# Kernel optimization log

Hardware: AMD Instinct MI355X
Metric: run time of the kernel (lower is better)

## Reference

```python
import jax, jax.numpy as jnp
import numpy as np

EPS = 1e-5


def setup_inputs() -> dict:
    key = jax.random.key(0)
    ks = jax.random.split(key, 10)
    B, C, H, W = 4, 256, 64, 64
    x = jax.random.normal(ks[0], (B, C, H, W), dtype=jnp.float32)
    s = 1.0 / np.sqrt(C)
    inp = {
        "x": x,
        "gn_w": jnp.ones((C,), jnp.float32),
        "gn_b": jnp.zeros((C,), jnp.float32),
        "wq": jax.random.normal(ks[1], (C, C), jnp.float32) * s,
        "bq": jnp.zeros((C,), jnp.float32),
        "wk": jax.random.normal(ks[2], (C, C), jnp.float32) * s,
        "bk": jnp.zeros((C,), jnp.float32),
        "wv": jax.random.normal(ks[3], (C, C), jnp.float32) * s,
        "bv": jnp.zeros((C,), jnp.float32),
        "wo": jax.random.normal(ks[4], (C, C), jnp.float32) * s,
        "bo": jnp.zeros((C,), jnp.float32),
    }
    return inp


def _forward(x, gn_w, gn_b, wq, bq, wk, bk, wv, bv, wo, bo):
    B, C, H, W = x.shape
    G = C // 2  # num_groups = channels // 2 -> 2 channels per group
    # GroupNorm
    xg = x.reshape(B, G, C // G, H, W)
    mu = jnp.mean(xg, axis=(2, 3, 4), keepdims=True)
    var = jnp.var(xg, axis=(2, 3, 4), keepdims=True)
    hn = ((xg - mu) * jax.lax.rsqrt(var + EPS)).reshape(B, C, H, W)
    hn = hn * gn_w[None, :, None, None] + gn_b[None, :, None, None]
    # tokens: (B, N, C), N = H*W
    h = hn.transpose(0, 2, 3, 1).reshape(B, H * W, C)
    q = h @ wq.T + bq
    k = h @ wk.T + bk
    v = h @ wv.T + bv
    # full NxN attention, scaled by C^-0.5 (as in original)
    scores = jnp.einsum("bnc,bmc->bnm", q, k) * (C ** -0.5)
    attn = jax.nn.softmax(scores, axis=-1)
    h2 = jnp.einsum("bnm,bmc->bnc", attn, v)  # (B, N, C)
    # faithful replication of the original's layout-scrambling reshape:
    # (B,N,C) -> (B,H,W,C) -> permute (B,C,H,W) -> reshape (B,HW,C)
    h2 = h2.reshape(B, H, W, C).transpose(0, 3, 1, 2).reshape(B, H * W, C)
    out = (h2 @ wo.T + bo).reshape(B, C, H, W)
    return x + out


def reference(x, gn_w, gn_b, wq, bq, wk, bk, wv, bv, wo, bo):
    return _forward(x, gn_w, gn_b, wq, bq, wk, bk, wv, bv, wo, bo)
```

## Files before the change

### kernel.cpp

```cpp
#include <hip/hip_runtime.h>

typedef unsigned short u16;
typedef unsigned int   u32;
typedef __attribute__((ext_vector_type(8)))  short short8;
typedef __attribute__((ext_vector_type(4)))  float f32x4;
typedef __attribute__((ext_vector_type(16))) float f32x16;

#define DI __device__ __forceinline__

DI u16 f2bf(float f){
  u32 u = __builtin_bit_cast(u32, f);
  u += 0x7fffu + ((u >> 16) & 1u);
  return (u16)(u >> 16);
}

DI void gl_lds16(const void* g, void* l){
  __builtin_amdgcn_global_load_lds((const __attribute__((address_space(1))) void*)g,
                                   (__attribute__((address_space(3))) void*)l, 16, 0, 0);
}

DI f32x4 mfma16(short8 a, short8 b, f32x4 c){
  return __builtin_amdgcn_mfma_f32_16x16x32_bf16(a, b, c, 0, 0, 0);
}
DI f32x16 mfma32(short8 a, short8 b, f32x16 c){
  return __builtin_amdgcn_mfma_f32_32x32x16_bf16(a, b, c, 0, 0, 0);
}
DI f32x16 z16(){
  f32x16 v;
  #pragma unroll
  for (int i=0;i<16;i++) v[i]=0.f;
  return v;
}

union U8 { u32 u[4]; short8 s; };

#define OFF_WBF   0u
#define OFF_STATS (512u<<10)
#define OFF_HTOK  (1u<<20)
#define OFF_Q     ((1u<<20) + (8u<<20))
#define OFF_K     ((1u<<20) + (16u<<20))
#define OFF_VT    ((1u<<20) + (24u<<20))
#define OFF_H2T   OFF_Q
#define OFF_PART  ((1u<<20) + (32u<<20))
#define OFF_ML    ((1u<<20) + (96u<<20))

__global__ void k_prep(const float* w0, const float* w1, const float* w2, const float* w3, u16* wbf){
  const float* src = (blockIdx.y==0)?w0:(blockIdx.y==1)?w1:(blockIdx.y==2)?w2:w3;
  u16* d = wbf + blockIdx.y*65536;
  int i = (blockIdx.x*256 + threadIdx.x)*4;
  float4 v = *(const float4*)(src + i);
  u32 lo = (u32)f2bf(v.x) | ((u32)f2bf(v.y)<<16);
  u32 hi = (u32)f2bf(v.z) | ((u32)f2bf(v.w)<<16);
  *(uint2*)(d + i) = make_uint2(lo, hi);
}

__global__ void k_gnstats(const float* x, float2* stats){
  int bg = blockIdx.x;
  const float* p = x + (size_t)bg*8192;
  float s = 0.f, ss = 0.f;
  #pragma unroll
  for (int i=0;i<8;i++){
    float4 v = *(const float4*)(p + threadIdx.x*4 + i*1024);
    s  += v.x+v.y+v.z+v.w;
    ss += v.x*v.x + v.y*v.y + v.z*v.z + v.w*v.w;
  }
  #pragma unroll
  for (int off=1; off<64; off<<=1){ s += __shfl_xor(s, off, 64); ss += __shfl_xor(ss, off, 64); }
  __shared__ float as[4], aq[4];
  int w = threadIdx.x>>6;
  if ((threadIdx.x&63)==0){ as[w]=s; aq[w]=ss; }
  __syncthreads();
  if (threadIdx.x==0){
    s = as[0]+as[1]+as[2]+as[3]; ss = aq[0]+aq[1]+aq[2]+aq[3];
    float mu = s * (1.f/8192.f);
    float var = ss * (1.f/8192.f) - mu*mu;
    stats[bg] = make_float2(mu, rsqrtf(var + 1e-5f));
  }
}

__global__ void k_gnapply(const float* x, const float* gw, const float* gb,
                          const float2* stats, u16* htok){
  __shared__ u16 tile[64*256];
  int b = blockIdx.y, n0 = blockIdx.x*64, t = threadIdx.x;
  const float* xb = x + (size_t)b*1048576;
  #pragma unroll
  for (int p=0;p<4;p++){
    int c = p*64 + (t>>2);
    float2 st = stats[b*128 + (c>>1)];
    float scl = st.y * gw[c];
    float off = gb[c] - st.x*scl;
    const float* src = xb + (size_t)c*4096 + n0 + (t&3)*16;
    #pragma unroll
    for (int u2=0;u2<4;u2++){
      float4 v = *(const float4*)(src + u2*4);
      float vv[4] = {v.x,v.y,v.z,v.w};
      #pragma unroll
      for (int j=0;j<4;j++){
        int n = (t&3)*16 + u2*4 + j;
        int addr = n*512 + ((c*2) ^ ((n&7)<<4));
        *(u16*)((char*)tile + addr) = f2bf(vv[j]*scl + off);
      }
    }
  }
  __syncthreads();
  int n = t>>2, seg = t&3;
  char* dst = (char*)(htok + ((size_t)(b*4096 + n0 + n)*256 + seg*64));
  #pragma unroll
  for (int i=0;i<8;i++){
    int boff = n*512 + (((seg*128) + i*16) ^ ((n&7)<<4));
    *(uint4*)(dst + i*16) = *(const uint4*)((const char*)tile + boff);
  }
}

DI void gemm_v2(const u16* Ag, const u16* Wg, int row0, int t,
                u16* lds_a, f32x4 acc[4][4]){
  const int w = t>>6, l = t&63, lo = l&15, hi = l>>4;
  const char* Ab = (const char*)Ag + (size_t)row0*512;
  #pragma unroll
  for (int i=0;i<8;i++){
    int row = w*16 + i*2 + (l>>5);
    gl_lds16(Ab + row*512 + (((l&31)*16) ^ ((row&7)<<4)), lds_a + w*4096 + i*512);
  }
  __syncthreads();
  const char* Wb = (const char*)Wg;
  #pragma unroll
  for (int dk=0; dk<4; dk++){
    #pragma unroll
    for (int s=0;s<2;s++){
      short8 af[4], bf[4];
      #pragma unroll
      for (int cf=0;cf<4;cf++){
        int col = w*64 + cf*16 + lo;
        bf[cf] = *(const short8*)(Wb + (size_t)col*512 + dk*128 + s*64 + hi*16);
      }
      #pragma unroll
      for (int rg=0;rg<4;rg++){
        int row = rg*16 + lo;
        af[rg] = *(const short8*)((const char*)lds_a + row*512 + ((dk*128 + s*64 + hi*16) ^ ((row&7)<<4)));
      }
      #pragma unroll
      for (int rg=0;rg<4;rg++)
        #pragma unroll
        for (int cf=0;cf<4;cf++)
          acc[rg][cf] = mfma16(af[rg], bf[cf], acc[rg][cf]);
    }
  }
}

__global__ __launch_bounds__(256,2) void k_qkv(const u16* htok, const u16* wbf,
    const float* bq, const float* bk, const float* bv,
    u16* qo, u16* ko, u16* vt){
  __shared__ u16 lds_a[64*256];
  const int t = threadIdx.x, mode = blockIdx.y, row0 = blockIdx.x*64;
  const u16* W = wbf + mode*65536;
  const float* bias = (mode==0)?bq:((mode==1)?bk:bv);
  f32x4 acc[4][4];
  #pragma unroll
  for (int i=0;i<4;i++)
    #pragma unroll
    for (int j=0;j<4;j++) acc[i][j] = (f32x4){0.f,0.f,0.f,0.f};
  gemm_v2(htok, W, row0, t, lds_a, acc);
  const int w = t>>6, l = t&63, lo = l&15, hi = l>>4;
  if (mode < 2){
    float scl = (mode==0)? 0.09016844f : 1.0f;
    u16* dst = (mode==0)? qo : ko;
    #pragma unroll
    for (int rg=0;rg<4;rg++)
      #pragma unroll
      for (int cf=0;cf<4;cf++){
        int col = w*64 + cf*16 + lo;
        float bs = bias[col];
        #pragma unroll
        for (int r=0;r<4;r++){
          int grow = row0 + rg*16 + hi*4 + r;
          dst[(size_t)grow*256 + col] = f2bf((acc[rg][cf][r] + bs)*scl);
        }
      }
  } else {
    __syncthreads();
    #pragma unroll
    for (int rg=0;rg<4;rg++)
      #pragma unroll
      for (int cf=0;cf<4;cf++){
        int col = w*64 + cf*16 + lo;
        float bs = bias[col];
        ushort4 pk;
        pk.x = f2bf(acc[rg][cf][0]+bs); pk.y = f2bf(acc[rg][cf][1]+bs);
        pk.z = f2bf(acc[rg][cf][2]+bs); pk.w = f2bf(acc[rg][cf][3]+bs);
        int rl = rg*16 + hi*4;
        int addr = col*128 + ((rl*2) ^ ((col&7)<<4));
        *(ushort4*)((char*)lds_a + addr) = pk;
      }
    __syncthreads();
    int b = row0 >> 12, nb = row0 & 4095;
    #pragma unroll
    for (int p=0;p<8;p++){
      int c = p*32 + (t>>3), i = t&7;
      uint4 vd = *(const uint4*)((const char*)lds_a + c*128 + ((i*16) ^ ((c&7)<<4)));
      *(uint4*)((char*)vt + ((size_t)(b*256 + c)*4096 + nb)*2 + i*16) = vd;
    }
  }
}

__global__ __launch_bounds__(256,2) void k_out(const u16* h2t, const u16* wo,
    const float* bo, const float* x, float* out){
  __shared__ u16 lds_a[64*256];
  const int t = threadIdx.x, row0 = blockIdx.x*64;
  f32x4 acc[4][4];
  #pragma unroll
  for (int i=0;i<4;i++)
    #pragma unroll
    for (int j=0;j<4;j++) acc[i][j] = (f32x4){0.f,0.f,0.f,0.f};
  gemm_v2(h2t, wo, row0, t, lds_a, acc);
  const int w = t>>6, l = t&63, lo = l&15, hi = l>>4;
  #pragma unroll
  for (int rg=0;rg<4;rg++)
    #pragma unroll
    for (int cf=0;cf<4;cf++){
      int col = w*64 + cf*16 + lo;
      float bs = bo[col];
      #pragma unroll
      for (int r=0;r<4;r++){
        size_t flat = (size_t)(row0 + rg*16 + hi*4 + r)*256 + col;
        out[flat] = x[flat] + acc[rg][cf][r] + bs;
      }
    }
}

__global__ __launch_bounds__(512,2) void k_attn(const u16* q, const u16* k,
                                                const u16* vt, u16* part, float2* ml){
  __shared__ char smem[131072];
  const int t = threadIdx.x, w = t>>6, l = t&63;
  const int lq = l&31, h = l>>5;
  const int bid = blockIdx.x;
  const int x = bid&7, idx = bid>>3;
  const int combo = x*2 + (idx&1);
  const int b = combo>>2, ks = combo&3, qt = idx>>1;

  const char* kg = (const char*)k  + ((size_t)b*4096 + (size_t)ks*1024)*512;
  const char* vg = (const char*)vt + (size_t)b*2097152 + (size_t)ks*2048;

  short8 qf[16];
  {
    const char* qrow = (const char*)q + ((size_t)b*4096 + qt*256 + w*32 + lq)*512;
    #pragma unroll
    for (int dk=0;dk<16;dk++) qf[dk] = *(const short8*)(qrow + dk*32 + h*16);
  }

  f32x16 O[8];
  #pragma unroll
  for (int ct=0;ct<8;ct++) O[ct] = z16();
  float m_run = -1e30f, l_run = 0.f;

  auto stage = [&](int ti, int buf){
    #pragma unroll
    for (int sub=0; sub<2; ++sub){
      char* kd = smem + buf*32768 + sub*16384;
      char* vd = smem + 65536 + buf*32768 + sub*16384;
      #pragma unroll
      for (int j=0;j<2;j++){
        int key = w*4 + j*2 + h;
        gl_lds16(kg + (size_t)(ti*64 + sub*32 + key)*512 + (((l&31)*16) ^ ((key&7)<<4)),
                 kd + (w*2+j)*1024);
      }
      #pragma unroll
      for (int j=0;j<2;j++){
        int c = w*32 + j*16 + (l>>2);
        gl_lds16(vg + (size_t)c*8192 + ti*128 + sub*64 + (((l&3)*16) ^ (((l>>3)&3)<<4)),
                 vd + (w*2+j)*1024);
      }
    }
  };

  auto smpv = [&](const f32x16& S, const char* vbuf){
    float pmax = S[0];
    #pragma unroll
    for (int r=1;r<16;r++) pmax = fmaxf(pmax, S[r]);
    pmax = fmaxf(pmax, __shfl_xor(pmax, 32, 64));
    if (__any(pmax > m_run + 8.f)){
      float mn = fmaxf(m_run, pmax);
      float sclq = exp2f(m_run - mn);
      m_run = mn;
      l_run *= sclq;
      #pragma unroll
      for (int r=0;r<16;r++){
        float sr = __shfl(sclq, (r&3)+8*(r>>2)+4*h, 64);
        #pragma unroll
        for (int ct=0;ct<8;ct++) O[ct][r] *= sr;
      }
    }
    float p[16]; float ps = 0.f;
    #pragma unroll
    for (int r=0;r<16;r++){ p[r] = exp2f(S[r] - m_run); ps += p[r]; }
    l_run += ps + __shfl_xor(ps, 32, 64);
    u32 pk[8];
    #pragma unroll
    for (int j=0;j<8;j++){
      u32 u0 = __builtin_bit_cast(u32, p[2*j]);
      u32 u1 = __builtin_bit_cast(u32, p[2*j+1]);
      pk[j] = (u1 & 0xffff0000u) | (u0 >> 16);
    }
    #pragma unroll
    for (int kc=0;kc<2;kc++){
      u32 sA = h ? pk[4*kc]   : pk[4*kc+2];
      u32 sB = h ? pk[4*kc+1] : pk[4*kc+3];
      u32 xA = __shfl_xor(sA, 32, 64);
      u32 xB = __shfl_xor(sB, 32, 64);
      U8 pa;
      pa.u[0] = h ? xA : pk[4*kc];
      pa.u[1] = h ? xB : pk[4*kc+1];
      pa.u[2] = h ? pk[4*kc+2] : xA;
      pa.u[3] = h ? pk[4*kc+3] : xB;
      __builtin_amdgcn_s_setprio(1);
      #pragma unroll
      for (int ct=0;ct<8;ct++){
        short8 vb = *(const short8*)(vbuf + (size_t)(ct*32+lq)*64 + ((kc*32 + h*16) ^ (((lq>>1)&3)<<4)));
        O[ct] = mfma32(pa.s, vb, O[ct]);
      }
      __builtin_amdgcn_s_setprio(0);
    }
  };

  stage(0, 0);
  __syncthreads();

  for (int tile=0; tile<16; ++tile){
    const int cur = tile&1;
    if (tile < 15) stage(tile+1, cur^1);
    const char* kbuf0 = smem + cur*32768;
    const char* kbuf1 = kbuf0 + 16384;
    const char* vbuf0 = smem + 65536 + cur*32768;
    const char* vbuf1 = vbuf0 + 16384;

    f32x16 S0 = z16(), S1 = z16();
    __builtin_amdgcn_s_setprio(1);
    #pragma unroll
    for (int dk=0;dk<16;dk++){
      int dby = (dk*32 + h*16) ^ ((lq&7)<<4);
      short8 k0 = *(const short8*)(kbuf0 + (size_t)lq*512 + dby);
      short8 k1 = *(const short8*)(kbuf1 + (size_t)lq*512 + dby);
      S0 = mfma32(k0, qf[dk], S0);
      S1 = mfma32(k1, qf[dk], S1);
    }
    __builtin_amdgcn_s_setprio(0);

    smpv(S0, vbuf0);
    smpv(S1, vbuf1);
    __syncthreads();
  }

  if (h == 0)
    ml[(size_t)combo*4096 + qt*256 + w*32 + lq] = make_float2(m_run, l_run);
  u16* otile = (u16*)smem;
  char* pbase = (char*)part + ((size_t)combo*4096 + (size_t)qt*256)*512;
  #pragma unroll
  for (int rd=0; rd<2; ++rd){
    __syncthreads();
    if ((w>>2) == rd){
      int wl = w&3;
      #pragma unroll
      for (int ct=0;ct<8;ct++)
        #pragma unroll
        for (int r=0;r<16;r++){
          int row = wl*32 + (r&3) + 8*(r>>2) + 4*h;
          otile[row*256 + ct*32 + lq] = f2bf(O[ct][r]);
        }
    }
    __syncthreads();
    const char* sb2 = (const char*)smem;
    char* gb2 = pbase + (size_t)rd*65536;
    #pragma unroll
    for (int j=0;j<8;j++)
      *(uint4*)(gb2 + t*16 + (size_t)j*8192) = *(const uint4*)(sb2 + t*16 + (size_t)j*8192);
  }
}

__global__ __launch_bounds__(256,2) void k_combine(const u16* part, const float2* ml, u16* h2t){
  __shared__ u16 tile[64*256];
  const int t = threadIdx.x, b = blockIdx.y, n0 = blockIdx.x*64;
  const int n = t>>2, cc = (t&3)*64;
  const int gn = n0 + n;
  float2 st[4]; float ms = -1e30f;
  #pragma unroll
  for (int ksi=0;ksi<4;ksi++){ st[ksi] = ml[(size_t)(b*4+ksi)*4096 + gn]; ms = fmaxf(ms, st[ksi].x); }
  float wn[4]; float denom = 0.f;
  #pragma unroll
  for (int ksi=0;ksi<4;ksi++){ wn[ksi] = exp2f(st[ksi].x - ms); denom += wn[ksi]*st[ksi].y; }
  float inv = 1.f/denom;
  #pragma unroll
  for (int ksi=0;ksi<4;ksi++) wn[ksi] *= inv;
  float acc[64];
  #pragma unroll
  for (int j=0;j<64;j++) acc[j] = 0.f;
  #pragma unroll
  for (int ksi=0;ksi<4;ksi++){
    const u16* src = part + ((size_t)(b*4+ksi)*4096 + gn)*256 + cc;
    float wv = wn[ksi];
    #pragma unroll
    for (int j8=0;j8<8;j8++){
      short8 v = *(const short8*)(src + j8*8);
      #pragma unroll
      for (int e=0;e<8;e++){
        u32 uu = ((u32)(u16)v[e])<<16;
        acc[j8*8+e] += wv * __builtin_bit_cast(float, uu);
      }
    }
  }
  char* tb = (char*)tile;
  #pragma unroll
  for (int j=0;j<32;j++){
    u32 pkv = ((u32)f2bf(acc[2*j+1])<<16) | f2bf(acc[2*j]);
    *(u32*)(tb + n*512 + ((cc*2 + j*4) ^ ((n&7)<<4))) = pkv;
  }
  __syncthreads();
  {
    const char* tbc = (const char*)tile;
    u32 outw[32];
    #pragma unroll
    for (int j=0;j<32;j++){
      u16 v0 = *(const u16*)(tbc + (2*j  )*512 + ((t*2) ^ (((2*j  )&7)<<4)));
      u16 v1 = *(const u16*)(tbc + (2*j+1)*512 + ((t*2) ^ (((2*j+1)&7)<<4)));
      outw[j] = ((u32)v1<<16) | v0;
    }
    char* dst = (char*)h2t + ((size_t)(b*256 + t)*4096 + n0)*2;
    #pragma unroll
    for (int j=0;j<8;j++){
      uint4 vv; vv.x = outw[4*j]; vv.y = outw[4*j+1]; vv.z = outw[4*j+2]; vv.w = outw[4*j+3];
      *(uint4*)(dst + j*16) = vv;
    }
  }
}

extern "C" void kernel_launch(void* const* d_in, const int* in_sizes, int n_in,
                              void* d_out, int out_size, void* d_ws, size_t ws_size,
                              hipStream_t stream) {
  const float* x    = (const float*)d_in[0];
  const float* gn_w = (const float*)d_in[1];
  const float* gn_b = (const float*)d_in[2];
  const float* wq   = (const float*)d_in[3];
  const float* bq   = (const float*)d_in[4];
  const float* wk   = (const float*)d_in[5];
  const float* bk   = (const float*)d_in[6];
  const float* wv   = (const float*)d_in[7];
  const float* bv   = (const float*)d_in[8];
  const float* wo   = (const float*)d_in[9];
  const float* bo   = (const float*)d_in[10];
  float* out = (float*)d_out;
  char* ws = (char*)d_ws;

  u16*    wbf   = (u16*)(ws + OFF_WBF);
  float2* stats = (float2*)(ws + OFF_STATS);
  u16*    htok  = (u16*)(ws + OFF_HTOK);
  u16*    qb    = (u16*)(ws + OFF_Q);
  u16*    kb    = (u16*)(ws + OFF_K);
  u16*    vt    = (u16*)(ws + OFF_VT);
  u16*    h2t   = (u16*)(ws + OFF_H2T);
  u16*    part  = (u16*)(ws + OFF_PART);
  float2* ml    = (float2*)(ws + OFF_ML);

  k_prep   <<<dim3(64,4), 256, 0, stream>>>(wq, wk, wv, wo, wbf);
  k_gnstats<<<512,        256, 0, stream>>>(x, stats);
  k_gnapply<<<dim3(64,4), 256, 0, stream>>>(x, gn_w, gn_b, stats, htok);
  k_qkv    <<<dim3(256,3),256, 0, stream>>>(htok, wbf, bq, bk, bv, qb, kb, vt);
  k_attn   <<<256,        512, 0, stream>>>(qb, kb, vt, part, ml);
  k_combine<<<dim3(64,4), 256, 0, stream>>>(part, ml, h2t);
  k_out    <<<256,        256, 0, stream>>>(h2t, wbf + 3*65536, bo, x, out);
}
```

Measured before the change: 169.2 us.

## Fuse Q/K/V projections into one block per row tile; merge attention softmax over two sub-tiles

The QKV kernel now loads each 64-row activation tile into LDS once and computes all three projections in sequence, instead of launching three separate blocks that each reload the same tile. The grid shrinks from 768 to 256 blocks. In attention, the two 32-key sub-tiles share a single running-max check and rescale, and all PV MFMAs are issued back to back. This cuts redundant loads, branches and shuffles per tile, but the QKV launch now has less parallelism and each block does serial work.

```diff
diff --git a/kernel.cpp b/kernel.cpp
--- a/kernel.cpp
+++ b/kernel.cpp
@@ -112,17 +112,124 @@
   }
 }
 
-DI void gemm_v2(const u16* Ag, const u16* Wg, int row0, int t,
-                u16* lds_a, f32x4 acc[4][4]){
+__global__ __launch_bounds__(256,2) void k_qkv(const u16* htok, const u16* wbf,
+    const float* bq, const float* bk, const float* bv,
+    u16* qo, u16* ko, u16* vt){
+  __shared__ u16 lds_a[64*256];
+  const int t = threadIdx.x, row0 = blockIdx.x*64;
   const int w = t>>6, l = t&63, lo = l&15, hi = l>>4;
-  const char* Ab = (const char*)Ag + (size_t)row0*512;
-  #pragma unroll
-  for (int i=0;i<8;i++){
-    int row = w*16 + i*2 + (l>>5);
-    gl_lds16(Ab + row*512 + (((l&31)*16) ^ ((row&7)<<4)), lds_a + w*4096 + i*512);
-  }
+  {
+    const char* Ab = (const char*)htok + (size_t)row0*512;
+    #pragma unroll
+    for (int i=0;i<8;i++){
+      int row = w*16 + i*2 + (l>>5);
+      gl_lds16(Ab + row*512 + (((l&31)*16) ^ ((row&7)<<4)), lds_a + w*4096 + i*512);
+    }
+    __syncthreads();
+  }
+  auto compute = [&](const u16* W, f32x4 acc[4][4]){
+    #pragma unroll
+    for (int i=0;i<4;i++)
+      #pragma unroll
+      for (int j=0;j<4;j++) acc[i][j] = (f32x4){0.f,0.f,0.f,0.f};
+    const char* Wb = (const char*)W;
+    #pragma unroll
+    for (int dk=0; dk<4; dk++){
+      #pragma unroll
+      for (int s=0;s<2;s++){
+        short8 af[4], bf[4];
+        #pragma unroll
+        for (int cf=0;cf<4;cf++){
+          int col = w*64 + cf*16 + lo;
+          bf[cf] = *(const short8*)(Wb + (size_t)col*512 + dk*128 + s*64 + hi*16);
+        }
+        #pragma unroll
+        for (int rg=0;rg<4;rg++){
+          int row = rg*16 + lo;
+          af[rg] = *(const short8*)((const char*)lds_a + row*512 + ((dk*128 + s*64 + hi*16) ^ ((row&7)<<4)));
+        }
+        #pragma unroll
+        for (int rg=0;rg<4;rg++)
+          #pragma unroll
+          for (int cf=0;cf<4;cf++)
+            acc[rg][cf] = mfma16(af[rg], bf[cf], acc[rg][cf]);
+      }
+    }
+  };
+  f32x4 acc[4][4];
+  compute(wbf, acc);
+  #pragma unroll
+  for (int rg=0;rg<4;rg++)
+    #pragma unroll
+    for (int cf=0;cf<4;cf++){
+      int col = w*64 + cf*16 + lo;
+      float bs = bq[col];
+      #pragma unroll
+      for (int r=0;r<4;r++){
+        int grow = row0 + rg*16 + hi*4 + r;
+        qo[(size_t)grow*256 + col] = f2bf((acc[rg][cf][r] + bs)*0.09016844f);
+      }
+    }
+  compute(wbf + 65536, acc);
+  #pragma unroll
+  for (int rg=0;rg<4;rg++)
+    #pragma unroll
+    for (int cf=0;cf<4;cf++){
+      int col = w*64 + cf*16 + lo;
+      float bs = bk[col];
+      #pragma unroll
+      for (int r=0;r<4;r++){
+        int grow = row0 + rg*16 + hi*4 + r;
+        ko[(size_t)grow*256 + col] = f2bf(acc[rg][cf][r] + bs);
+      }
+    }
+  compute(wbf + 2*65536, acc);
   __syncthreads();
-  const char* Wb = (const char*)Wg;
+  #pragma unroll
+  for (int rg=0;rg<4;rg++)
+    #pragma unroll
+    for (int cf=0;cf<4;cf++){
+      int col = w*64 + cf*16 + lo;
+      float bs = bv[col];
+      ushort4 pk;
+      pk.x = f2bf(acc[rg][cf][0]+bs); pk.y = f2bf(acc[rg][cf][1]+bs);
+      pk.z = f2bf(acc[rg][cf][2]+bs); pk.w = f2bf(acc[rg][cf][3]+bs);
+      int rl = rg*16 + hi*4;
+      int addr = col*128 + ((rl*2) ^ ((col&7)<<4));
+      *(ushort4*)((char*)lds_a + addr) = pk;
+    }
+  __syncthreads();
+  {
+    int b = row0 >> 12, nb = row0 & 4095;
+    #pragma unroll
+    for (int p=0;p<8;p++){
+      int c = p*32 + (t>>3), i = t&7;
+      uint4 vd = *(const uint4*)((const char*)lds_a + c*128 + ((i*16) ^ ((c&7)<<4)));
+      *(uint4*)((char*)vt + ((size_t)(b*256 + c)*4096 + nb)*2 + i*16) = vd;
+    }
+  }
+}
+
+__global__ __launch_bounds__(256,2) void k_out(const u16* h2t, const u16* wo,
+    const float* bo, const float* x, float* out){
+  __shared__ u16 lds_a[64*256];
+  const int t = threadIdx.x, row0 = blockIdx.x*64;
+  const int w = t>>6, l = t&63, lo = l&15, hi = l>>4;
+  {
+    const char* Ab = (const char*)h2t + (size_t)row0*512;
+    #pragma unroll
+    for (int i=0;i<8;i++){
+      int row = w*16 + i*2 + (l>>5);
+      gl_lds16(Ab + row*512 + (((l&31)*16) ^ ((row&7)<<4)), lds_a + w*4096 + i*512);
+    }
+    __syncthreads();
+  }
+  f32x4 acc[4][4];
+  #pragma unroll
+  for (int i=0;i<4;i++)
+    #pragma unroll
+    for (int j=0;j<4;j++) acc[i][j] = (f32x4){0.f,0.f,0.f,0.f};
+  const char* Wb = (const char*)wo;
   #pragma unroll
   for (int dk=0; dk<4; dk++){
     #pragma unroll
@@ -145,74 +252,6 @@
           acc[rg][cf] = mfma16(af[rg], bf[cf], acc[rg][cf]);
     }
   }
-}
-
-__global__ __launch_bounds__(256,2) void k_qkv(const u16* htok, const u16* wbf,
-    const float* bq, const float* bk, const float* bv,
-    u16* qo, u16* ko, u16* vt){
-  __shared__ u16 lds_a[64*256];
-  const int t = threadIdx.x, mode = blockIdx.y, row0 = blockIdx.x*64;
-  const u16* W = wbf + mode*65536;
-  const float* bias = (mode==0)?bq:((mode==1)?bk:bv);
-  f32x4 acc[4][4];
-  #pragma unroll
-  for (int i=0;i<4;i++)
-    #pragma unroll
-    for (int j=0;j<4;j++) acc[i][j] = (f32x4){0.f,0.f,0.f,0.f};
-  gemm_v2(htok, W, row0, t, lds_a, acc);
-  const int w = t>>6, l = t&63, lo = l&15, hi = l>>4;
-  if (mode < 2){
-    float scl = (mode==0)? 0.09016844f : 1.0f;
-    u16* dst = (mode==0)? qo : ko;
-    #pragma unroll
-    for (int rg=0;rg<4;rg++)
-      #pragma unroll
-      for (int cf=0;cf<4;cf++){
-        int col = w*64 + cf*16 + lo;
-        float bs = bias[col];
-        #pragma unroll
-        for (int r=0;r<4;r++){
-          int grow = row0 + rg*16 + hi*4 + r;
-          dst[(size_t)grow*256 + col] = f2bf((acc[rg][cf][r] + bs)*scl);
-        }
-      }
-  } else {
-    __syncthreads();
-    #pragma unroll
-    for (int rg=0;rg<4;rg++)
-      #pragma unroll
-      for (int cf=0;cf<4;cf++){
-        int col = w*64 + cf*16 + lo;
-        float bs = bias[col];
-        ushort4 pk;
-        pk.x = f2bf(acc[rg][cf][0]+bs); pk.y = f2bf(acc[rg][cf][1]+bs);
-        pk.z = f2bf(acc[rg][cf][2]+bs); pk.w = f2bf(acc[rg][cf][3]+bs);
-        int rl = rg*16 + hi*4;
-        int addr = col*128 + ((rl*2) ^ ((col&7)<<4));
-        *(ushort4*)((char*)lds_a + addr) = pk;
-      }
-    __syncthreads();
-    int b = row0 >> 12, nb = row0 & 4095;
-    #pragma unroll
-    for (int p=0;p<8;p++){
-      int c = p*32 + (t>>3), i = t&7;
-      uint4 vd = *(const uint4*)((const char*)lds_a + c*128 + ((i*16) ^ ((c&7)<<4)));
-      *(uint4*)((char*)vt + ((size_t)(b*256 + c)*4096 + nb)*2 + i*16) = vd;
-    }
-  }
-}
-
-__global__ __launch_bounds__(256,2) void k_out(const u16* h2t, const u16* wo,
-    const float* bo, const float* x, float* out){
-  __shared__ u16 lds_a[64*256];
-  const int t = threadIdx.x, row0 = blockIdx.x*64;
-  f32x4 acc[4][4];
-  #pragma unroll
-  for (int i=0;i<4;i++)
-    #pragma unroll
-    for (int j=0;j<4;j++) acc[i][j] = (f32x4){0.f,0.f,0.f,0.f};
-  gemm_v2(h2t, wo, row0, t, lds_a, acc);
-  const int w = t>>6, l = t&63, lo = l&15, hi = l>>4;
   #pragma unroll
   for (int rg=0;rg<4;rg++)
     #pragma unroll
@@ -272,55 +311,6 @@
     }
   };
 
-  auto smpv = [&](const f32x16& S, const char* vbuf){
-    float pmax = S[0];
-    #pragma unroll
-    for (int r=1;r<16;r++) pmax = fmaxf(pmax, S[r]);
-    pmax = fmaxf(pmax, __shfl_xor(pmax, 32, 64));
-    if (__any(pmax > m_run + 8.f)){
-      float mn = fmaxf(m_run, pmax);
-      float sclq = exp2f(m_run - mn);
-      m_run = mn;
-      l_run *= sclq;
-      #pragma unroll
-      for (int r=0;r<16;r++){
-        float sr = __shfl(sclq, (r&3)+8*(r>>2)+4*h, 64);
-        #pragma unroll
-        for (int ct=0;ct<8;ct++) O[ct][r] *= sr;
-      }
-    }
-    float p[16]; float ps = 0.f;
-    #pragma unroll
-    for (int r=0;r<16;r++){ p[r] = exp2f(S[r] - m_run); ps += p[r]; }
-    l_run += ps + __shfl_xor(ps, 32, 64);
-    u32 pk[8];
-    #pragma unroll
-    for (int j=0;j<8;j++){
-      u32 u0 = __builtin_bit_cast(u32, p[2*j]);
-      u32 u1 = __builtin_bit_cast(u32, p[2*j+1]);
-      pk[j] = (u1 & 0xffff0000u) | (u0 >> 16);
-    }
-    #pragma unroll
-    for (int kc=0;kc<2;kc++){
-      u32 sA = h ? pk[4*kc]   : pk[4*kc+2];
-      u32 sB = h ? pk[4*kc+1] : pk[4*kc+3];
-      u32 xA = __shfl_xor(sA, 32, 64);
-      u32 xB = __shfl_xor(sB, 32, 64);
-      U8 pa;
-      pa.u[0] = h ? xA : pk[4*kc];
-      pa.u[1] = h ? xB : pk[4*kc+1];
-      pa.u[2] = h ? pk[4*kc+2] : xA;
-      pa.u[3] = h ? pk[4*kc+3] : xB;
-      __builtin_amdgcn_s_setprio(1);
-      #pragma unroll
-      for (int ct=0;ct<8;ct++){
-        short8 vb = *(const short8*)(vbuf + (size_t)(ct*32+lq)*64 + ((kc*32 + h*16) ^ (((lq>>1)&3)<<4)));
-        O[ct] = mfma32(pa.s, vb, O[ct]);
-      }
-      __builtin_amdgcn_s_setprio(0);
-    }
-  };
-
   stage(0, 0);
   __syncthreads();
 
@@ -344,8 +334,84 @@
     }
     __builtin_amdgcn_s_setprio(0);
 
-    smpv(S0, vbuf0);
-    smpv(S1, vbuf1);
+    float pmax = fmaxf(S0[0], S1[0]);
+    #pragma unroll
+    for (int r=1;r<16;r++) pmax = fmaxf(pmax, fmaxf(S0[r], S1[r]));
+    pmax = fmaxf(pmax, __shfl_xor(pmax, 32, 64));
+    if (__any(pmax > m_run + 8.f)){
+      float mn = fmaxf(m_run, pmax);
+      float sclq = exp2f(m_run - mn);
+      m_run = mn;
+      l_run *= sclq;
+      #pragma unroll
+      for (int r=0;r<16;r++){
+        float sr = __shfl(sclq, (r&3)+8*(r>>2)+4*h, 64);
+        #pragma unroll
+        for (int ct=0;ct<8;ct++) O[ct][r] *= sr;
+      }
+    }
+    float ps = 0.f;
+    u32 pk0[8], pk1[8];
+    #pragma unroll
+    for (int j=0;j<8;j++){
+      float p0 = exp2f(S0[2*j]   - m_run);
+      float p1 = exp2f(S0[2*j+1] - m_run);
+      ps += p0 + p1;
+      pk0[j] = (__builtin_bit_cast(u32, p1) & 0xffff0000u) | (__builtin_bit_cast(u32, p0) >> 16);
+    }
+    #pragma unroll
+    for (int j=0;j<8;j++){
+      float p0 = exp2f(S1[2*j]   - m_run);
+      float p1 = exp2f(S1[2*j+1] - m_run);
+      ps += p0 + p1;
+      pk1[j] = (__builtin_bit_cast(u32, p1) & 0xffff0000u) | (__builtin_bit_cast(u32, p0) >> 16);
+    }
+    l_run += ps + __shfl_xor(ps, 32, 64);
+
+    U8 pa00, pa01, pa10, pa11;
+    #pragma unroll
+    for (int kc=0;kc<2;kc++){
+      {
+        u32 sA = h ? pk0[4*kc]   : pk0[4*kc+2];
+        u32 sB = h ? pk0[4*kc+1] : pk0[4*kc+3];
+        u32 xA = __shfl_xor(sA, 32, 64);
+        u32 xB = __shfl_xor(sB, 32, 64);
+        U8& pa = kc ? pa01 : pa00;
+        pa.u[0] = h ? xA : pk0[4*kc];
+        pa.u[1] = h ? xB : pk0[4*kc+1];
+        pa.u[2] = h ? pk0[4*kc+2] : xA;
+        pa.u[3] = h ? pk0[4*kc+3] : xB;
+      }
+      {
+        u32 sA = h ? pk1[4*kc]   : pk1[4*kc+2];
+        u32 sB = h ? pk1[4*kc+1] : pk1[4*kc+3];
+        u32 xA = __shfl_xor(sA, 32, 64);
+        u32 xB = __shfl_xor(sB, 32, 64);
+        U8& pa = kc ? pa11 : pa10;
+        pa.u[0] = h ? xA : pk1[4*kc];
+        pa.u[1] = h ? xB : pk1[4*kc+1];
+        pa.u[2] = h ? pk1[4*kc+2] : xA;
+        pa.u[3] = h ? pk1[4*kc+3] : xB;
+      }
+    }
+    __builtin_amdgcn_s_setprio(1);
+    #pragma unroll
+    for (int kc=0;kc<2;kc++){
+      #pragma unroll
+      for (int ct=0;ct<8;ct++){
+        short8 vb = *(const short8*)(vbuf0 + (size_t)(ct*32+lq)*64 + ((kc*32 + h*16) ^ (((lq>>1)&3)<<4)));
+        O[ct] = mfma32(kc ? pa01.s : pa00.s, vb, O[ct]);
+      }
+    }
+    #pragma unroll
+    for (int kc=0;kc<2;kc++){
+      #pragma unroll
+      for (int ct=0;ct<8;ct++){
+        short8 vb = *(const short8*)(vbuf1 + (size_t)(ct*32+lq)*64 + ((kc*32 + h*16) ^ (((lq>>1)&3)<<4)));
+        O[ct] = mfma32(kc ? pa11.s : pa10.s, vb, O[ct]);
+      }
+    }
+    __builtin_amdgcn_s_setprio(0);
     __syncthreads();
   }
 
@@ -461,7 +527,7 @@
   k_prep   <<<dim3(64,4), 256, 0, stream>>>(wq, wk, wv, wo, wbf);
   k_gnstats<<<512,        256, 0, stream>>>(x, stats);
   k_gnapply<<<dim3(64,4), 256, 0, stream>>>(x, gn_w, gn_b, stats, htok);
-  k_qkv    <<<dim3(256,3),256, 0, stream>>>(htok, wbf, bq, bk, bv, qb, kb, vt);
+  k_qkv    <<<256,        256, 0, stream>>>(htok, wbf, bq, bk, bv, qb, kb, vt);
   k_attn   <<<256,        512, 0, stream>>>(qb, kb, vt, part, ml);
   k_combine<<<dim3(64,4), 256, 0, stream>>>(part, ml, h2t);
   k_out    <<<256,        256, 0, stream>>>(h2t, wbf + 3*65536, bo, x, out);
```

New measurement: 184.6 us. 9.1% more time.
